# Kernel optimization log

Measured on AMD Instinct MI355X. Metric: run time of the kernel, lower is better.

Reference implementation:

```python
import jax, jax.numpy as jnp
import numpy as np


def position_encoding(feature_size, d_model):
    pos = jnp.arange(feature_size, dtype=jnp.float32)[:, None]
    _2i = jnp.arange(0, d_model, 2, dtype=jnp.float32)
    ang = pos / jnp.power(10000.0, _2i / d_model)  # [F, D/2]
    pe = jnp.zeros((feature_size, d_model), dtype=jnp.float32)
    pe = pe.at[:, 0::2].set(jnp.sin(ang))
    pe = pe.at[:, 1::2].set(jnp.cos(ang))
    return pe


def setup_inputs() -> dict:
    key = jax.random.key(0)
    ks = jax.random.split(key, 11)
    B, F, D, T, V = 32, 512, 256, 32, 128
    sc = 0.02
    return {
        "f": jax.random.normal(ks[0], (B, F, D), dtype=jnp.float32),
        "decoder_input_ids": jax.random.randint(ks[1], (B, T), 0, V),
        "emb": sc * jax.random.normal(ks[2], (V, D), dtype=jnp.float32),
        "w_e": sc * jax.random.normal(ks[3], (D, D), dtype=jnp.float32),
        "w_h": sc * jax.random.normal(ks[4], (D, D), dtype=jnp.float32),
        "w_f": sc * jax.random.normal(ks[5], (D, D), dtype=jnp.float32),
        "w_q": sc * jax.random.normal(ks[6], (D, D), dtype=jnp.float32),
        "w_s": sc * jax.random.normal(ks[7], (D, D), dtype=jnp.float32),
        "w_g": sc * jax.random.normal(ks[8], (D, 2 * D), dtype=jnp.float32),
        "w_ih": sc * jax.random.normal(ks[9], (4 * D, 2 * D), dtype=jnp.float32),
        "w_hh": sc * jax.random.normal(ks[10], (4 * D, D), dtype=jnp.float32),
    }


def reference(f, decoder_input_ids, emb, w_e, w_h, w_f, w_q, w_s, w_g, w_ih, w_hh):
    B, F, D = f.shape
    q = position_encoding(F, D)                      # [F, D]
    dec = emb[decoder_input_ids]                     # [B, T, D]
    # loop-invariant attention terms, hoisted: w_f(f) + w_q(q)
    base = jnp.einsum('bfd,od->bfo', f, w_f) + (q @ w_q.T)[None]  # [B, F, D]
    fq = f + q[None]                                 # [B, F, D]

    def step(carry, x_t):
        h, cell, s, cp = carry
        # LSTMCell (bias=False), torch gate order i, f, g, o
        xin = jnp.concatenate([x_t, cp], axis=-1)    # [B, 2D]
        gates = xin @ w_ih.T + h @ w_hh.T            # [B, 4D]
        gi, gf, gg, go = jnp.split(gates, 4, axis=-1)
        cell = jax.nn.sigmoid(gf) * cell + jax.nn.sigmoid(gi) * jnp.tanh(gg)
        h = jax.nn.sigmoid(go) * jnp.tanh(cell)
        # Bahdanau-style energy; softmax over feature (last) dim per source
        t_in = jnp.tanh((h @ w_h.T)[:, None] + base + jnp.einsum('bfd,od->bfo', s, w_s))
        e = jnp.einsum('bfd,od->bfo', t_in, w_e)     # [B, F, D]
        alpha = jax.nn.softmax(e, axis=-1)
        s = s + alpha
        c = (alpha * f).sum(1)                       # [B, D]
        cp = (alpha * fq).sum(1)                     # [B, D]
        pred = jnp.concatenate([c, h], axis=-1) @ w_g.T  # [B, D]
        return (h, cell, s, cp), pred

    z = jnp.zeros((B, D), dtype=f.dtype)
    carry0 = (z, z, jnp.zeros_like(f), z)
    _, preds = jax.lax.scan(step, carry0, jnp.swapaxes(dec, 0, 1))  # [T, B, D]
    return jnp.swapaxes(preds, 0, 1)                 # [B, T, D]
```

## Files before the change

kernel.cpp:

```cpp
#include <hip/hip_runtime.h>
#include <math.h>

#define NB 32
#define NF 512
#define ND 256
#define NT 32
#define RPB 32
#define NTILE (NF / RPB)

typedef __attribute__((ext_vector_type(8))) short bf16x8;
typedef __attribute__((ext_vector_type(4))) float f32x4;

__device__ __forceinline__ float sigmoidf_(float x) { return 1.0f / (1.0f + __expf(-x)); }

__device__ __forceinline__ short f2bf(float x) {
    union { float f; unsigned u; } v; v.f = x;
    unsigned r = (v.u + 0x7FFF + ((v.u >> 16) & 1)) >> 16;
    return (short)r;
}

__global__ void pe_kernel(float* __restrict__ q) {
    int p = blockIdx.x;
    int d = threadIdx.x;
    float i2 = (float)((d >> 1) << 1);
    float rate = expf(-9.210340371976184f * (i2 / (float)ND));
    float ang = (float)p * rate;
    q[p * ND + d] = (d & 1) ? cosf(ang) : sinf(ang);
}

__global__ void gather_kernel(const int* __restrict__ ids, const float* __restrict__ emb,
                              float* __restrict__ dec) {
    int bt = blockIdx.x;
    int d = threadIdx.x;
    dec[(size_t)bt * ND + d] = emb[(size_t)ids[bt] * ND + d];
}

__global__ void wcvt_kernel(const float* __restrict__ w, short* __restrict__ wb, int n) {
    int i = blockIdx.x * 256 + threadIdx.x;
    if (i < n) wb[i] = f2bf(w[i]);
}

__global__ void qwq_kernel(const float* __restrict__ q, const float* __restrict__ w_q,
                           float* __restrict__ qwq) {
    int p = blockIdx.x;
    int o = threadIdx.x;
    __shared__ float qs[ND];
    qs[o] = q[(size_t)p * ND + o];
    __syncthreads();
    const float4* wr = (const float4*)(w_q + (size_t)o * ND);
    float acc = 0.f;
    for (int k4 = 0; k4 < ND / 4; ++k4) {
        float4 w = wr[k4];
        int k = 4 * k4;
        acc += qs[k] * w.x + qs[k + 1] * w.y + qs[k + 2] * w.z + qs[k + 3] * w.w;
    }
    qwq[(size_t)p * ND + o] = acc;
}

__global__ void base_kernel(const float* __restrict__ fin, const float* __restrict__ w_f,
                            const float* __restrict__ qwq, float* __restrict__ base) {
    int b = blockIdx.x / NTILE;
    int f0 = (blockIdx.x % NTILE) * RPB;
    int o = threadIdx.x;
    __shared__ float fs[RPB][ND];
    #pragma unroll
    for (int r = 0; r < RPB; ++r)
        fs[r][o] = fin[((size_t)(b * NF + f0 + r)) * ND + o];
    __syncthreads();
    float acc[RPB];
    #pragma unroll
    for (int r = 0; r < RPB; ++r) acc[r] = 0.f;
    const float4* wr = (const float4*)(w_f + (size_t)o * ND);
    for (int k4 = 0; k4 < ND / 4; ++k4) {
        float4 w = wr[k4];
        int k = 4 * k4;
        #pragma unroll
        for (int r = 0; r < RPB; ++r)
            acc[r] += fs[r][k] * w.x + fs[r][k + 1] * w.y + fs[r][k + 2] * w.z + fs[r][k + 3] * w.w;
    }
    #pragma unroll
    for (int r = 0; r < RPB; ++r)
        base[((size_t)(b * NF + f0 + r)) * ND + o] = acc[r] + qwq[(size_t)(f0 + r) * ND + o];
}

__global__ void prep_kernel(int t,
                            const float* __restrict__ dec,
                            const float* __restrict__ cpart, const float* __restrict__ cppart,
                            const float* __restrict__ h,
                            float* __restrict__ Z, float* __restrict__ ZP) {
    int b = blockIdx.x;
    int d = threadIdx.x;
    float csum = 0.f, cpsum = 0.f;
    if (t > 0) {
        for (int tile = 0; tile < NTILE; ++tile) {
            csum  += cpart [((size_t)tile * NB + b) * ND + d];
            cpsum += cppart[((size_t)tile * NB + b) * ND + d];
        }
    }
    float hv = h[(size_t)b * ND + d];
    float xv = (t < NT) ? dec[((size_t)b * NT + t) * ND + d] : 0.0f;
    Z[(size_t)b * 768 + d]       = xv;
    Z[(size_t)b * 768 + 256 + d] = cpsum;
    Z[(size_t)b * 768 + 512 + d] = hv;
    ZP[(size_t)b * 512 + d]       = csum;
    ZP[(size_t)b * 512 + 256 + d] = hv;
}

#define ZSTRIDE 769
#define ZPSTRIDE 513
__global__ void gates_kernel(int t, int mode,
                             const float* __restrict__ Z, const float* __restrict__ ZP,
                             const float* __restrict__ w_ih, const float* __restrict__ w_hh,
                             const float* __restrict__ w_g,
                             float* __restrict__ gatesT, float* __restrict__ out) {
    extern __shared__ float lds[];
    int bid = blockIdx.x;
    int tid = threadIdx.x;

    if (bid < 128) {
        if (!(mode & 1)) return;
        int j0 = bid * 8;
        float* wl = lds;
        float* zl = lds + 8 * 768;
        float4* wl4 = (float4*)wl;
        for (int cc = 0; cc < 6; ++cc) {
            int idx4 = tid + cc * 256;
            int flat = idx4 * 4;
            int r = flat / 768;
            int col = flat - r * 768;
            float4 v;
            if (col < 512) v = *(const float4*)(w_ih + (size_t)(j0 + r) * 512 + col);
            else           v = *(const float4*)(w_hh + (size_t)(j0 + r) * 256 + (col - 512));
            wl4[idx4] = v;
        }
        for (int b = 0; b < NB; ++b)
            for (int k = tid; k < 768; k += 256)
                zl[b * ZSTRIDE + k] = Z[(size_t)b * 768 + k];
        __syncthreads();
        int r = tid >> 5;
        int b = tid & 31;
        const float4* wr4 = (const float4*)(wl + r * 768);
        const float* zb = zl + b * ZSTRIDE;
        float acc = 0.f;
        #pragma unroll 8
        for (int k4 = 0; k4 < 192; ++k4) {
            float4 w = wr4[k4];
            int k = 4 * k4;
            acc += w.x * zb[k] + w.y * zb[k + 1] + w.z * zb[k + 2] + w.w * zb[k + 3];
        }
        gatesT[(size_t)(j0 + r) * NB + b] = acc;
    } else {
        if (!(mode & 2)) return;
        int p0 = (bid - 128) * 8;
        float* wl = lds;
        float* zl = lds + 8 * 512;
        float4* wl4 = (float4*)wl;
        for (int cc = 0; cc < 4; ++cc) {
            int idx4 = tid + cc * 256;
            int flat = idx4 * 4;
            int r = flat >> 9;
            int col = flat & 511;
            wl4[idx4] = *(const float4*)(w_g + (size_t)(p0 + r) * 512 + col);
        }
        for (int b = 0; b < NB; ++b)
            for (int k = tid; k < 512; k += 256)
                zl[b * ZPSTRIDE + k] = ZP[(size_t)b * 512 + k];
        __syncthreads();
        int r = tid >> 5;
        int b = tid & 31;
        const float4* wr4 = (const float4*)(wl + r * 512);
        const float* zb = zl + b * ZPSTRIDE;
        float acc = 0.f;
        #pragma unroll 8
        for (int k4 = 0; k4 < 128; ++k4) {
            float4 w = wr4[k4];
            int k = 4 * k4;
            acc += w.x * zb[k] + w.y * zb[k + 1] + w.z * zb[k + 2] + w.w * zb[k + 3];
        }
        out[((size_t)b * NT + (t - 1)) * ND + p0 + r] = acc;
    }
}

__global__ void cell_hwh_kernel(const float* __restrict__ gatesT,
                                float* __restrict__ h, float* __restrict__ cell,
                                const float* __restrict__ w_h, float* __restrict__ hwh) {
    int b = blockIdx.x;
    int o = threadIdx.x;
    __shared__ float hn[ND];
    float gi = gatesT[(size_t)(0 * ND + o) * NB + b];
    float gf = gatesT[(size_t)(1 * ND + o) * NB + b];
    float gg = gatesT[(size_t)(2 * ND + o) * NB + b];
    float go = gatesT[(size_t)(3 * ND + o) * NB + b];
    float cold = cell[(size_t)b * ND + o];
    float cnew = sigmoidf_(gf) * cold + sigmoidf_(gi) * tanhf(gg);
    float hval = sigmoidf_(go) * tanhf(cnew);
    cell[(size_t)b * ND + o] = cnew;
    h[(size_t)b * ND + o] = hval;
    hn[o] = hval;
    __syncthreads();
    const float4* whr = (const float4*)(w_h + (size_t)o * ND);
    float a = 0.f;
    for (int k4 = 0; k4 < ND / 4; ++k4) {
        float4 w = whr[k4]; int k = 4 * k4;
        a += hn[k] * w.x + hn[k + 1] * w.y + hn[k + 2] * w.z + hn[k + 3] * w.w;
    }
    hwh[(size_t)b * ND + o] = a;
}

__global__ void attn_step_kernel(const float* __restrict__ base, float* __restrict__ sws,
                                 const float* __restrict__ fin, const float* __restrict__ q,
                                 const float* __restrict__ hwh,
                                 const short* __restrict__ w_e_bf, const short* __restrict__ w_s_bf,
                                 float* __restrict__ cpart, float* __restrict__ cppart) {
    int b = blockIdx.x / NTILE;
    int tile = blockIdx.x % NTILE;
    int f0 = tile * RPB;
    int tid = threadIdx.x;
    int l = tid & 63;
    int wv = tid >> 6;

    __shared__ __align__(16) short tin_bf[RPB * ND];
    __shared__ float e_lds[RPB * 257];

    {
        float hv = hwh[(size_t)b * ND + tid];
        char* tb = (char*)tin_bf;
        #pragma unroll 8
        for (int r = 0; r < RPB; ++r) {
            size_t idx = ((size_t)(b * NF + f0 + r)) * ND + tid;
            float tv = tanhf(hv + base[idx] + sws[idx]);
            int byte = (r * 512 + tid * 2) ^ ((r & 7) << 4);
            *(short*)(tb + byte) = f2bf(tv);
        }
    }
    __syncthreads();

    int o0 = wv * 64;
    int arow_lo = l & 15, kgrp = (l >> 4) * 8;
    f32x4 acc[2][4];
    #pragma unroll
    for (int mt = 0; mt < 2; ++mt)
        #pragma unroll
        for (int nt = 0; nt < 4; ++nt)
            acc[mt][nt] = (f32x4)0.f;
    {
        const char* tb = (const char*)tin_bf;
        #pragma unroll
        for (int ks = 0; ks < 8; ++ks) {
            int kb = ks * 32 + kgrp;
            bf16x8 afr[2];
            #pragma unroll
            for (int mt = 0; mt < 2; ++mt) {
                int row = mt * 16 + arow_lo;
                int byte = (row * 512 + kb * 2) ^ ((row & 7) << 4);
                afr[mt] = *(const bf16x8*)(tb + byte);
            }
            #pragma unroll
            for (int nt = 0; nt < 4; ++nt) {
                int o = o0 + nt * 16 + arow_lo;
                bf16x8 bfr = *(const bf16x8*)(w_e_bf + (size_t)o * ND + kb);
                #pragma unroll
                for (int mt = 0; mt < 2; ++mt)
                    acc[mt][nt] = __builtin_amdgcn_mfma_f32_16x16x32_bf16(afr[mt], bfr, acc[mt][nt], 0, 0, 0);
            }
        }
    }
    {
        int crow = (l >> 4) * 4, ccol = l & 15;
        #pragma unroll
        for (int mt = 0; mt < 2; ++mt)
            #pragma unroll
            for (int nt = 0; nt < 4; ++nt) {
                int col = o0 + nt * 16 + ccol;
                #pragma unroll
                for (int reg = 0; reg < 4; ++reg)
                    e_lds[(mt * 16 + crow + reg) * 257 + col] = acc[mt][nt][reg];
            }
    }
    __syncthreads();

    {
        char* tb = (char*)tin_bf;
        for (int r = wv * 8; r < wv * 8 + 8; ++r) {
            float* er = e_lds + r * 257;
            float m = -1e30f;
            #pragma unroll
            for (int j = 0; j < 4; ++j) m = fmaxf(m, er[l + 64 * j]);
            #pragma unroll
            for (int off = 32; off >= 1; off >>= 1) m = fmaxf(m, __shfl_xor(m, off));
            float ssum = 0.f;
            float ev[4];
            #pragma unroll
            for (int j = 0; j < 4; ++j) {
                ev[j] = __expf(er[l + 64 * j] - m);
                ssum += ev[j];
            }
            #pragma unroll
            for (int off = 32; off >= 1; off >>= 1) ssum += __shfl_xor(ssum, off);
            float inv = 1.0f / ssum;
            #pragma unroll
            for (int j = 0; j < 4; ++j) {
                float a = ev[j] * inv;
                int kk = l + 64 * j;
                er[kk] = a;
                int byte = (r * 512 + kk * 2) ^ ((r & 7) << 4);
                *(short*)(tb + byte) = f2bf(a);
            }
        }
    }
    __syncthreads();

    {
        float pc = 0.f, pcp = 0.f;
        #pragma unroll 8
        for (int r = 0; r < RPB; ++r) {
            float a = e_lds[r * 257 + tid];
            size_t idx = ((size_t)(b * NF + f0 + r)) * ND + tid;
            float fv = fin[idx];
            float qv = q[(size_t)(f0 + r) * ND + tid];
            pc += a * fv;
            pcp += a * (fv + qv);
        }
        cpart [((size_t)tile * NB + b) * ND + tid] = pc;
        cppart[((size_t)tile * NB + b) * ND + tid] = pcp;
    }

    {
        f32x4 acc2[2][4];
        #pragma unroll
        for (int mt = 0; mt < 2; ++mt)
            #pragma unroll
            for (int nt = 0; nt < 4; ++nt)
                acc2[mt][nt] = (f32x4)0.f;
        const char* tb = (const char*)tin_bf;
        #pragma unroll
        for (int ks = 0; ks < 8; ++ks) {
            int kb = ks * 32 + kgrp;
            bf16x8 afr[2];
            #pragma unroll
            for (int mt = 0; mt < 2; ++mt) {
                int row = mt * 16 + arow_lo;
                int byte = (row * 512 + kb * 2) ^ ((row & 7) << 4);
                afr[mt] = *(const bf16x8*)(tb + byte);
            }
            #pragma unroll
            for (int nt = 0; nt < 4; ++nt) {
                int o = o0 + nt * 16 + arow_lo;
                bf16x8 bfr = *(const bf16x8*)(w_s_bf + (size_t)o * ND + kb);
                #pragma unroll
                for (int mt = 0; mt < 2; ++mt)
                    acc2[mt][nt] = __builtin_amdgcn_mfma_f32_16x16x32_bf16(afr[mt], bfr, acc2[mt][nt], 0, 0, 0);
            }
        }
        int crow = (l >> 4) * 4, ccol = l & 15;
        #pragma unroll
        for (int mt = 0; mt < 2; ++mt)
            #pragma unroll
            for (int nt = 0; nt < 4; ++nt) {
                int col = o0 + nt * 16 + ccol;
                #pragma unroll
                for (int reg = 0; reg < 4; ++reg) {
                    int row = mt * 16 + crow + reg;
                    size_t idx = ((size_t)(b * NF + f0 + row)) * ND + col;
                    sws[idx] += acc2[mt][nt][reg];
                }
            }
    }
}

extern "C" void kernel_launch(void* const* d_in, const int* in_sizes, int n_in,
                              void* d_out, int out_size, void* d_ws, size_t ws_size,
                              hipStream_t stream) {
    const float* fin  = (const float*)d_in[0];
    const int*   ids  = (const int*)  d_in[1];
    const float* emb  = (const float*)d_in[2];
    const float* w_e  = (const float*)d_in[3];
    const float* w_h  = (const float*)d_in[4];
    const float* w_f  = (const float*)d_in[5];
    const float* w_q  = (const float*)d_in[6];
    const float* w_s  = (const float*)d_in[7];
    const float* w_g  = (const float*)d_in[8];
    const float* w_ih = (const float*)d_in[9];
    const float* w_hh = (const float*)d_in[10];
    float* out = (float*)d_out;
    float* ws  = (float*)d_ws;

    size_t off = 0;
    float* q      = ws + off; off += (size_t)NF * ND;
    float* scratch= ws + off; off += (size_t)NF * ND;
    float* dec    = ws + off; off += (size_t)NB * NT * ND;
    float* base   = ws + off; off += (size_t)NB * NF * ND;
    float* sws    = ws + off; off += (size_t)NB * NF * ND;
    float* h      = ws + off; off += (size_t)NB * ND;
    float* cell   = ws + off; off += (size_t)NB * ND;
    float* hwh    = ws + off; off += (size_t)NB * ND;
    float* cpart  = ws + off; off += (size_t)NTILE * NB * ND;
    float* cppart = ws + off; off += (size_t)NTILE * NB * ND;
    short* w_e_bf = (short*)(ws + off); off += (size_t)ND * ND / 2;
    short* w_s_bf = (short*)(ws + off); off += (size_t)ND * ND / 2;

    float* qwq    = scratch;
    float* Z      = scratch;
    float* ZP     = scratch + 24576;
    float* gatesT = scratch + 24576 + 16384;

    hipMemsetAsync(sws, 0, sizeof(float) * (size_t)NB * NF * ND, stream);
    hipMemsetAsync(h, 0, sizeof(float) * NB * ND, stream);
    hipMemsetAsync(cell, 0, sizeof(float) * NB * ND, stream);

    pe_kernel<<<NF, ND, 0, stream>>>(q);
    gather_kernel<<<NB * NT, ND, 0, stream>>>(ids, emb, dec);
    wcvt_kernel<<<ND * ND / 256, 256, 0, stream>>>(w_e, w_e_bf, ND * ND);
    wcvt_kernel<<<ND * ND / 256, 256, 0, stream>>>(w_s, w_s_bf, ND * ND);
    qwq_kernel<<<NF, ND, 0, stream>>>(q, w_q, qwq);
    base_kernel<<<NB * NTILE, ND, 0, stream>>>(fin, w_f, qwq, base);

    const size_t gates_lds = (size_t)(8 * 768 + NB * ZSTRIDE) * sizeof(float);

    for (int t = 0; t < NT; ++t) {
        int mode = (t > 0) ? 3 : 1;
        prep_kernel<<<NB, ND, 0, stream>>>(t, dec, cpart, cppart, h, Z, ZP);
        gates_kernel<<<160, ND, gates_lds, stream>>>(t, mode, Z, ZP, w_ih, w_hh, w_g, gatesT, out);
        cell_hwh_kernel<<<NB, ND, 0, stream>>>(gatesT, h, cell, w_h, hwh);
        attn_step_kernel<<<NB * NTILE, ND, 0, stream>>>(base, sws, fin, q, hwh,
                                                        w_e_bf, w_s_bf, cpart, cppart);
    }
    prep_kernel<<<NB, ND, 0, stream>>>(NT, dec, cpart, cppart, h, Z, ZP);
    gates_kernel<<<160, ND, gates_lds, stream>>>(NT, 2, Z, ZP, w_ih, w_hh, w_g, gatesT, out);
}
```

Baseline: 3.139 ms.

## Fold attention state into one buffer, fuse softmax in registers, drop prep kernel

Merges the loop-invariant base term and the running s·w_s accumulator into a single bsum buffer that is read once and written once per step, instead of reading base and sws and then doing a read-modify-write on sws. Softmax now runs directly on the MFMA accumulator registers, with cross-lane shuffles and a small LDS reduction, so the e_lds staging buffer goes away. It also drops the max subtraction, which leans on the energies staying small. The prep kernel is removed: the gates kernel sums the c and cp partials itself, adding redundant partial-sum reads in every block in exchange for one fewer launch per step.

```diff
diff --git a/kernel.cpp b/kernel.cpp
--- a/kernel.cpp
+++ b/kernel.cpp
@@ -58,7 +58,7 @@
 }
 
 __global__ void base_kernel(const float* __restrict__ fin, const float* __restrict__ w_f,
-                            const float* __restrict__ qwq, float* __restrict__ base) {
+                            const float* __restrict__ qwq, float* __restrict__ bsum) {
     int b = blockIdx.x / NTILE;
     int f0 = (blockIdx.x % NTILE) * RPB;
     int o = threadIdx.x;
@@ -80,36 +80,15 @@
     }
     #pragma unroll
     for (int r = 0; r < RPB; ++r)
-        base[((size_t)(b * NF + f0 + r)) * ND + o] = acc[r] + qwq[(size_t)(f0 + r) * ND + o];
-}
-
-__global__ void prep_kernel(int t,
-                            const float* __restrict__ dec,
-                            const float* __restrict__ cpart, const float* __restrict__ cppart,
-                            const float* __restrict__ h,
-                            float* __restrict__ Z, float* __restrict__ ZP) {
-    int b = blockIdx.x;
-    int d = threadIdx.x;
-    float csum = 0.f, cpsum = 0.f;
-    if (t > 0) {
-        for (int tile = 0; tile < NTILE; ++tile) {
-            csum  += cpart [((size_t)tile * NB + b) * ND + d];
-            cpsum += cppart[((size_t)tile * NB + b) * ND + d];
-        }
-    }
-    float hv = h[(size_t)b * ND + d];
-    float xv = (t < NT) ? dec[((size_t)b * NT + t) * ND + d] : 0.0f;
-    Z[(size_t)b * 768 + d]       = xv;
-    Z[(size_t)b * 768 + 256 + d] = cpsum;
-    Z[(size_t)b * 768 + 512 + d] = hv;
-    ZP[(size_t)b * 512 + d]       = csum;
-    ZP[(size_t)b * 512 + 256 + d] = hv;
+        bsum[((size_t)(b * NF + f0 + r)) * ND + o] = acc[r] + qwq[(size_t)(f0 + r) * ND + o];
 }
 
 #define ZSTRIDE 769
 #define ZPSTRIDE 513
 __global__ void gates_kernel(int t, int mode,
-                             const float* __restrict__ Z, const float* __restrict__ ZP,
+                             const float* __restrict__ dec,
+                             const float* __restrict__ cpart, const float* __restrict__ cppart,
+                             const float* __restrict__ h,
                              const float* __restrict__ w_ih, const float* __restrict__ w_hh,
                              const float* __restrict__ w_g,
                              float* __restrict__ gatesT, float* __restrict__ out) {
@@ -133,9 +112,20 @@
             else           v = *(const float4*)(w_hh + (size_t)(j0 + r) * 256 + (col - 512));
             wl4[idx4] = v;
         }
-        for (int b = 0; b < NB; ++b)
-            for (int k = tid; k < 768; k += 256)
-                zl[b * ZSTRIDE + k] = Z[(size_t)b * 768 + k];
+        for (int b = 0; b < NB; ++b) {
+            int d = tid;
+            float xv = (t < NT) ? dec[((size_t)b * NT + t) * ND + d] : 0.f;
+            float cpsum = 0.f;
+            if (t > 0) {
+                #pragma unroll
+                for (int tl = 0; tl < NTILE; ++tl)
+                    cpsum += cppart[((size_t)tl * NB + b) * ND + d];
+            }
+            float hv = h[(size_t)b * ND + d];
+            zl[b * ZSTRIDE + d]       = xv;
+            zl[b * ZSTRIDE + 256 + d] = cpsum;
+            zl[b * ZSTRIDE + 512 + d] = hv;
+        }
         __syncthreads();
         int r = tid >> 5;
         int b = tid & 31;
@@ -162,9 +152,14 @@
             int col = flat & 511;
             wl4[idx4] = *(const float4*)(w_g + (size_t)(p0 + r) * 512 + col);
         }
-        for (int b = 0; b < NB; ++b)
-            for (int k = tid; k < 512; k += 256)
-                zl[b * ZPSTRIDE + k] = ZP[(size_t)b * 512 + k];
+        for (int b = 0; b < NB; ++b) {
+            float csum = 0.f;
+            #pragma unroll
+            for (int tl = 0; tl < NTILE; ++tl)
+                csum += cpart[((size_t)tl * NB + b) * ND + tid];
+            zl[b * ZPSTRIDE + tid]       = csum;
+            zl[b * ZPSTRIDE + 256 + tid] = h[(size_t)b * ND + tid];
+        }
         __syncthreads();
         int r = tid >> 5;
         int b = tid & 31;
@@ -207,7 +202,7 @@
     hwh[(size_t)b * ND + o] = a;
 }
 
-__global__ void attn_step_kernel(const float* __restrict__ base, float* __restrict__ sws,
+__global__ void attn_step_kernel(float* __restrict__ bsum,
                                  const float* __restrict__ fin, const float* __restrict__ q,
                                  const float* __restrict__ hwh,
                                  const short* __restrict__ w_e_bf, const short* __restrict__ w_s_bf,
@@ -220,149 +215,199 @@
     int wv = tid >> 6;
 
     __shared__ __align__(16) short tin_bf[RPB * ND];
-    __shared__ float e_lds[RPB * 257];
-
+    __shared__ float sred[RPB][5];
+
+    int o0 = wv * 64;
+    int c15 = l & 15;
+    int g = l >> 4;
+    int kgrp = g * 8;
+    char* tb = (char*)tin_bf;
+
+    float bsv[2][4][4];
     {
-        float hv = hwh[(size_t)b * ND + tid];
-        char* tb = (char*)tin_bf;
-        #pragma unroll 8
-        for (int r = 0; r < RPB; ++r) {
-            size_t idx = ((size_t)(b * NF + f0 + r)) * ND + tid;
-            float tv = tanhf(hv + base[idx] + sws[idx]);
-            int byte = (r * 512 + tid * 2) ^ ((r & 7) << 4);
-            *(short*)(tb + byte) = f2bf(tv);
-        }
-    }
-    __syncthreads();
-
-    int o0 = wv * 64;
-    int arow_lo = l & 15, kgrp = (l >> 4) * 8;
+        float hv4[4];
+        #pragma unroll
+        for (int nt = 0; nt < 4; ++nt)
+            hv4[nt] = hwh[(size_t)b * ND + o0 + nt * 16 + c15];
+        #pragma unroll
+        for (int mt = 0; mt < 2; ++mt)
+            #pragma unroll
+            for (int reg = 0; reg < 4; ++reg) {
+                int r = mt * 16 + g * 4 + reg;
+                size_t rowb = ((size_t)(b * NF + f0 + r)) * ND;
+                #pragma unroll
+                for (int nt = 0; nt < 4; ++nt) {
+                    int col = o0 + nt * 16 + c15;
+                    float bs = bsum[rowb + col];
+                    bsv[mt][nt][reg] = bs;
+                    float tv = tanhf(hv4[nt] + bs);
+                    int byte = (r * 512 + col * 2) ^ ((r & 7) << 4);
+                    *(short*)(tb + byte) = f2bf(tv);
+                }
+            }
+    }
+    __syncthreads();
+
     f32x4 acc[2][4];
     #pragma unroll
     for (int mt = 0; mt < 2; ++mt)
         #pragma unroll
         for (int nt = 0; nt < 4; ++nt)
             acc[mt][nt] = (f32x4)0.f;
+    #pragma unroll
+    for (int ks = 0; ks < 8; ++ks) {
+        int kb = ks * 32 + kgrp;
+        bf16x8 afr[2];
+        #pragma unroll
+        for (int mt = 0; mt < 2; ++mt) {
+            int row = mt * 16 + c15;
+            int byte = (row * 512 + kb * 2) ^ ((row & 7) << 4);
+            afr[mt] = *(const bf16x8*)(tb + byte);
+        }
+        #pragma unroll
+        for (int nt = 0; nt < 4; ++nt) {
+            int o = o0 + nt * 16 + c15;
+            bf16x8 bfr = *(const bf16x8*)(w_e_bf + (size_t)o * ND + kb);
+            #pragma unroll
+            for (int mt = 0; mt < 2; ++mt)
+                acc[mt][nt] = __builtin_amdgcn_mfma_f32_16x16x32_bf16(afr[mt], bfr, acc[mt][nt], 0, 0, 0);
+        }
+    }
+
+    float ps[2][4];
+    #pragma unroll
+    for (int mt = 0; mt < 2; ++mt)
+        #pragma unroll
+        for (int reg = 0; reg < 4; ++reg) ps[mt][reg] = 0.f;
+    #pragma unroll
+    for (int mt = 0; mt < 2; ++mt)
+        #pragma unroll
+        for (int nt = 0; nt < 4; ++nt)
+            #pragma unroll
+            for (int reg = 0; reg < 4; ++reg) {
+                float a = __expf(acc[mt][nt][reg]);
+                acc[mt][nt][reg] = a;
+                ps[mt][reg] += a;
+            }
+    #pragma unroll
+    for (int off = 1; off <= 8; off <<= 1)
+        #pragma unroll
+        for (int mt = 0; mt < 2; ++mt)
+            #pragma unroll
+            for (int reg = 0; reg < 4; ++reg)
+                ps[mt][reg] += __shfl_xor(ps[mt][reg], off);
+    if (c15 == 0) {
+        #pragma unroll
+        for (int mt = 0; mt < 2; ++mt)
+            #pragma unroll
+            for (int reg = 0; reg < 4; ++reg)
+                sred[mt * 16 + g * 4 + reg][wv] = ps[mt][reg];
+    }
+    __syncthreads();
+    float inv[2][4];
+    #pragma unroll
+    for (int mt = 0; mt < 2; ++mt)
+        #pragma unroll
+        for (int reg = 0; reg < 4; ++reg) {
+            int r = mt * 16 + g * 4 + reg;
+            inv[mt][reg] = 1.0f / (sred[r][0] + sred[r][1] + sred[r][2] + sred[r][3]);
+        }
+    #pragma unroll
+    for (int mt = 0; mt < 2; ++mt)
+        #pragma unroll
+        for (int nt = 0; nt < 4; ++nt)
+            #pragma unroll
+            for (int reg = 0; reg < 4; ++reg)
+                acc[mt][nt][reg] *= inv[mt][reg];
+
     {
-        const char* tb = (const char*)tin_bf;
+        float pc[4], pcp[4];
+        #pragma unroll
+        for (int nt = 0; nt < 4; ++nt) { pc[nt] = 0.f; pcp[nt] = 0.f; }
+        #pragma unroll
+        for (int mt = 0; mt < 2; ++mt)
+            #pragma unroll
+            for (int reg = 0; reg < 4; ++reg) {
+                int r = mt * 16 + g * 4 + reg;
+                size_t rowb = ((size_t)(b * NF + f0 + r)) * ND;
+                size_t qrowb = (size_t)(f0 + r) * ND;
+                #pragma unroll
+                for (int nt = 0; nt < 4; ++nt) {
+                    int col = o0 + nt * 16 + c15;
+                    float a = acc[mt][nt][reg];
+                    float fv = fin[rowb + col];
+                    float qv = q[qrowb + col];
+                    pc[nt] += a * fv;
+                    pcp[nt] += a * (fv + qv);
+                }
+            }
+        #pragma unroll
+        for (int off = 16; off <= 32; off <<= 1)
+            #pragma unroll
+            for (int nt = 0; nt < 4; ++nt) {
+                pc[nt]  += __shfl_xor(pc[nt], off);
+                pcp[nt] += __shfl_xor(pcp[nt], off);
+            }
+        if (g == 0) {
+            #pragma unroll
+            for (int nt = 0; nt < 4; ++nt) {
+                int col = o0 + nt * 16 + c15;
+                cpart [((size_t)tile * NB + b) * ND + col] = pc[nt];
+                cppart[((size_t)tile * NB + b) * ND + col] = pcp[nt];
+            }
+        }
+    }
+
+    #pragma unroll
+    for (int mt = 0; mt < 2; ++mt)
+        #pragma unroll
+        for (int reg = 0; reg < 4; ++reg) {
+            int r = mt * 16 + g * 4 + reg;
+            #pragma unroll
+            for (int nt = 0; nt < 4; ++nt) {
+                int col = o0 + nt * 16 + c15;
+                int byte = (r * 512 + col * 2) ^ ((r & 7) << 4);
+                *(short*)(tb + byte) = f2bf(acc[mt][nt][reg]);
+            }
+        }
+    __syncthreads();
+
+    {
+        f32x4 acc2[2][4];
+        #pragma unroll
+        for (int mt = 0; mt < 2; ++mt)
+            #pragma unroll
+            for (int nt = 0; nt < 4; ++nt)
+                acc2[mt][nt] = (f32x4)0.f;
         #pragma unroll
         for (int ks = 0; ks < 8; ++ks) {
             int kb = ks * 32 + kgrp;
             bf16x8 afr[2];
             #pragma unroll
             for (int mt = 0; mt < 2; ++mt) {
-                int row = mt * 16 + arow_lo;
+                int row = mt * 16 + c15;
                 int byte = (row * 512 + kb * 2) ^ ((row & 7) << 4);
                 afr[mt] = *(const bf16x8*)(tb + byte);
             }
             #pragma unroll
             for (int nt = 0; nt < 4; ++nt) {
-                int o = o0 + nt * 16 + arow_lo;
-                bf16x8 bfr = *(const bf16x8*)(w_e_bf + (size_t)o * ND + kb);
-                #pragma unroll
-                for (int mt = 0; mt < 2; ++mt)
-                    acc[mt][nt] = __builtin_amdgcn_mfma_f32_16x16x32_bf16(afr[mt], bfr, acc[mt][nt], 0, 0, 0);
-            }
-        }
-    }
-    {
-        int crow = (l >> 4) * 4, ccol = l & 15;
-        #pragma unroll
-        for (int mt = 0; mt < 2; ++mt)
-            #pragma unroll
-            for (int nt = 0; nt < 4; ++nt) {
-                int col = o0 + nt * 16 + ccol;
-                #pragma unroll
-                for (int reg = 0; reg < 4; ++reg)
-                    e_lds[(mt * 16 + crow + reg) * 257 + col] = acc[mt][nt][reg];
-            }
-    }
-    __syncthreads();
-
-    {
-        char* tb = (char*)tin_bf;
-        for (int r = wv * 8; r < wv * 8 + 8; ++r) {
-            float* er = e_lds + r * 257;
-            float m = -1e30f;
-            #pragma unroll
-            for (int j = 0; j < 4; ++j) m = fmaxf(m, er[l + 64 * j]);
-            #pragma unroll
-            for (int off = 32; off >= 1; off >>= 1) m = fmaxf(m, __shfl_xor(m, off));
-            float ssum = 0.f;
-            float ev[4];
-            #pragma unroll
-            for (int j = 0; j < 4; ++j) {
-                ev[j] = __expf(er[l + 64 * j] - m);
-                ssum += ev[j];
-            }
-            #pragma unroll
-            for (int off = 32; off >= 1; off >>= 1) ssum += __shfl_xor(ssum, off);
-            float inv = 1.0f / ssum;
-            #pragma unroll
-            for (int j = 0; j < 4; ++j) {
-                float a = ev[j] * inv;
-                int kk = l + 64 * j;
-                er[kk] = a;
-                int byte = (r * 512 + kk * 2) ^ ((r & 7) << 4);
-                *(short*)(tb + byte) = f2bf(a);
-            }
-        }
-    }
-    __syncthreads();
-
-    {
-        float pc = 0.f, pcp = 0.f;
-        #pragma unroll 8
-        for (int r = 0; r < RPB; ++r) {
-            float a = e_lds[r * 257 + tid];
-            size_t idx = ((size_t)(b * NF + f0 + r)) * ND + tid;
-            float fv = fin[idx];
-            float qv = q[(size_t)(f0 + r) * ND + tid];
-            pc += a * fv;
-            pcp += a * (fv + qv);
-        }
-        cpart [((size_t)tile * NB + b) * ND + tid] = pc;
-        cppart[((size_t)tile * NB + b) * ND + tid] = pcp;
-    }
-
-    {
-        f32x4 acc2[2][4];
-        #pragma unroll
-        for (int mt = 0; mt < 2; ++mt)
-            #pragma unroll
-            for (int nt = 0; nt < 4; ++nt)
-                acc2[mt][nt] = (f32x4)0.f;
-        const char* tb = (const char*)tin_bf;
-        #pragma unroll
-        for (int ks = 0; ks < 8; ++ks) {
-            int kb = ks * 32 + kgrp;
-            bf16x8 afr[2];
-            #pragma unroll
-            for (int mt = 0; mt < 2; ++mt) {
-                int row = mt * 16 + arow_lo;
-                int byte = (row * 512 + kb * 2) ^ ((row & 7) << 4);
-                afr[mt] = *(const bf16x8*)(tb + byte);
-            }
-            #pragma unroll
-            for (int nt = 0; nt < 4; ++nt) {
-                int o = o0 + nt * 16 + arow_lo;
+                int o = o0 + nt * 16 + c15;
                 bf16x8 bfr = *(const bf16x8*)(w_s_bf + (size_t)o * ND + kb);
                 #pragma unroll
                 for (int mt = 0; mt < 2; ++mt)
                     acc2[mt][nt] = __builtin_amdgcn_mfma_f32_16x16x32_bf16(afr[mt], bfr, acc2[mt][nt], 0, 0, 0);
             }
         }
-        int crow = (l >> 4) * 4, ccol = l & 15;
-        #pragma unroll
-        for (int mt = 0; mt < 2; ++mt)
-            #pragma unroll
-            for (int nt = 0; nt < 4; ++nt) {
-                int col = o0 + nt * 16 + ccol;
+        #pragma unroll
+        for (int mt = 0; mt < 2; ++mt)
+            #pragma unroll
+            for (int reg = 0; reg < 4; ++reg) {
+                int r = mt * 16 + g * 4 + reg;
+                size_t rowb = ((size_t)(b * NF + f0 + r)) * ND;
                 #pragma unroll
-                for (int reg = 0; reg < 4; ++reg) {
-                    int row = mt * 16 + crow + reg;
-                    size_t idx = ((size_t)(b * NF + f0 + row)) * ND + col;
-                    sws[idx] += acc2[mt][nt][reg];
+                for (int nt = 0; nt < 4; ++nt) {
+                    int col = o0 + nt * 16 + c15;
+                    bsum[rowb + col] = bsv[mt][nt][reg] + acc2[mt][nt][reg];
                 }
             }
     }
@@ -389,8 +434,7 @@
     float* q      = ws + off; off += (size_t)NF * ND;
     float* scratch= ws + off; off += (size_t)NF * ND;
     float* dec    = ws + off; off += (size_t)NB * NT * ND;
-    float* base   = ws + off; off += (size_t)NB * NF * ND;
-    float* sws    = ws + off; off += (size_t)NB * NF * ND;
+    float* bsum   = ws + off; off += (size_t)NB * NF * ND;
     float* h      = ws + off; off += (size_t)NB * ND;
     float* cell   = ws + off; off += (size_t)NB * ND;
     float* hwh    = ws + off; off += (size_t)NB * ND;
@@ -400,11 +444,8 @@
     short* w_s_bf = (short*)(ws + off); off += (size_t)ND * ND / 2;
 
     float* qwq    = scratch;
-    float* Z      = scratch;
-    float* ZP     = scratch + 24576;
-    float* gatesT = scratch + 24576 + 16384;
-
-    hipMemsetAsync(sws, 0, sizeof(float) * (size_t)NB * NF * ND, stream);
+    float* gatesT = scratch + 65536;
+
     hipMemsetAsync(h, 0, sizeof(float) * NB * ND, stream);
     hipMemsetAsync(cell, 0, sizeof(float) * NB * ND, stream);
 
@@ -413,18 +454,18 @@
     wcvt_kernel<<<ND * ND / 256, 256, 0, stream>>>(w_e, w_e_bf, ND * ND);
     wcvt_kernel<<<ND * ND / 256, 256, 0, stream>>>(w_s, w_s_bf, ND * ND);
     qwq_kernel<<<NF, ND, 0, stream>>>(q, w_q, qwq);
-    base_kernel<<<NB * NTILE, ND, 0, stream>>>(fin, w_f, qwq, base);
+    base_kernel<<<NB * NTILE, ND, 0, stream>>>(fin, w_f, qwq, bsum);
 
     const size_t gates_lds = (size_t)(8 * 768 + NB * ZSTRIDE) * sizeof(float);
 
     for (int t = 0; t < NT; ++t) {
         int mode = (t > 0) ? 3 : 1;
-        prep_kernel<<<NB, ND, 0, stream>>>(t, dec, cpart, cppart, h, Z, ZP);
-        gates_kernel<<<160, ND, gates_lds, stream>>>(t, mode, Z, ZP, w_ih, w_hh, w_g, gatesT, out);
+        gates_kernel<<<160, ND, gates_lds, stream>>>(t, mode, dec, cpart, cppart, h,
+                                                     w_ih, w_hh, w_g, gatesT, out);
         cell_hwh_kernel<<<NB, ND, 0, stream>>>(gatesT, h, cell, w_h, hwh);
-        attn_step_kernel<<<NB * NTILE, ND, 0, stream>>>(base, sws, fin, q, hwh,
+        attn_step_kernel<<<NB * NTILE, ND, 0, stream>>>(bsum, fin, q, hwh,
                                                         w_e_bf, w_s_bf, cpart, cppart);
     }
-    prep_kernel<<<NB, ND, 0, stream>>>(NT, dec, cpart, cppart, h, Z, ZP);
-    gates_kernel<<<160, ND, gates_lds, stream>>>(NT, 2, Z, ZP, w_ih, w_hh, w_g, gatesT, out);
-}
+    gates_kernel<<<160, ND, gates_lds, stream>>>(NT, 2, dec, cpart, cppart, h,
+                                                 w_ih, w_hh, w_g, gatesT, out);
+}
```

Measured after the change: 3.050 ms. 2.8% less time.
